# Performance work log

Hardware: AMD Instinct MI355X
Metric: run time of the kernel (lower is better)

Reference implementation:

```python
import jax, jax.numpy as jnp
import numpy as np

B, S, D = 4, 4096, 1024
H = 16
DH = D // H  # 64, required by the fused kernel


def setup_inputs() -> dict:
    key = jax.random.key(0)
    ks = jax.random.split(key, 5)
    scale = 1.0 / np.sqrt(D)  # xavier-ish init scale for square matrices
    return {
        "x": jax.random.normal(ks[0], (B, S, D), dtype=jnp.float32),
        "Wq": jax.random.normal(ks[1], (D, D), dtype=jnp.float32) * scale,
        "Wk": jax.random.normal(ks[2], (D, D), dtype=jnp.float32) * scale,
        "Wv": jax.random.normal(ks[3], (D, D), dtype=jnp.float32) * scale,
        "Wo": jax.random.normal(ks[4], (D, D), dtype=jnp.float32) * scale,
    }


def reference(x, Wq, Wk, Wv, Wo):
    # Fused QKV projection + linear (non-softmax) attention.
    # Q = x Wq, K = x Wk, V = x Wv, split into H heads of size DH.
    b, s, d = x.shape
    h, dh = H, d // H

    def to_heads(t):
        return t.reshape(b, s, h, dh).transpose(0, 2, 1, 3)  # [B,H,S,dh]

    q = to_heads(jnp.einsum("bsd,de->bse", x, Wq))
    k = to_heads(jnp.einsum("bsd,de->bse", x, Wk))
    v = to_heads(jnp.einsum("bsd,de->bse", x, Wv))

    # Linear attention: O(S * dh^2) per head, never materializes [S,S].
    # out = (1/sqrt(dh)) * Q @ (K^T V)
    scale = 1.0 / jnp.sqrt(jnp.asarray(dh, dtype=x.dtype))
    kv = jnp.einsum("bhsd,bhse->bhde", k, v)          # [B,H,dh,dh]
    out = jnp.einsum("bhsd,bhde->bhse", q, kv) * scale  # [B,H,S,dh]

    # kernel output [B,H,S,dh] -> transpose(1,2) -> view [B,S,D]
    out = out.transpose(0, 2, 1, 3).reshape(b, s, d)
    # out_proj: nn.Linear(D, D, bias=False) -> x @ W.T
    return jnp.einsum("bsd,ed->bse", out, Wo)
```

## Files before the change

### kernel.cpp

```cpp
#include <hip/hip_runtime.h>

typedef unsigned short u16;
typedef unsigned int u32;
typedef u16 u16x8 __attribute__((ext_vector_type(8)));
typedef u16 u16x4 __attribute__((ext_vector_type(4)));
typedef __bf16 bf16x8 __attribute__((ext_vector_type(8)));
typedef float f32x4 __attribute__((ext_vector_type(4)));

__device__ __forceinline__ u16 f2bf(float f) {
    u32 u = __builtin_bit_cast(u32, f);
    u32 r = (u + 0x7fffu + ((u >> 16) & 1u)) >> 16;
    return (u16)r;
}
__device__ __forceinline__ void async16(const u16* g, u16* lds_base) {
    __builtin_amdgcn_global_load_lds(
        (const __attribute__((address_space(1))) void*)g,
        (__attribute__((address_space(3))) void*)lds_base, 16, 0, 0);
}
template <bool SW>
__device__ __forceinline__ f32x4 mf(bf16x8 a, bf16x8 b, f32x4 c) {
    if constexpr (SW) return __builtin_amdgcn_mfma_f32_16x16x32_bf16(b, a, c, 0, 0, 0);
    else              return __builtin_amdgcn_mfma_f32_16x16x32_bf16(a, b, c, 0, 0, 0);
}

#define BAR __builtin_amdgcn_s_barrier()
#define WAITLGK do { asm volatile("s_waitcnt lgkmcnt(0)" ::: "memory"); \
                     __builtin_amdgcn_sched_barrier(0); } while (0)
#define PRIO1 __builtin_amdgcn_s_setprio(1)
#define PRIO0 __builtin_amdgcn_s_setprio(0)
#define VM(n) asm volatile("s_waitcnt vmcnt(" #n ")" ::: "memory")

__global__ void xpose_cvt(const float* __restrict__ x, u16* __restrict__ xb,
                          u16* __restrict__ xbT) {
    __shared__ u16 tile[32][33];
    const int s0 = blockIdx.y * 32, n0 = blockIdx.x * 32;
    const int tx = threadIdx.x, ty = threadIdx.y;
#pragma unroll
    for (int r = 0; r < 4; ++r) {
        const int s = s0 + ty + 8 * r;
        const u16 bv = f2bf(x[(size_t)s * 1024 + n0 + tx]);
        xb[(size_t)s * 1024 + n0 + tx] = bv;
        tile[ty + 8 * r][tx] = bv;
    }
    __syncthreads();
    const int b = s0 >> 12;
    const int sl = s0 & 4095;
#pragma unroll
    for (int r = 0; r < 4; ++r) {
        const int n = n0 + ty + 8 * r;
        xbT[((size_t)b * 1024 + n) * 4096 + sl + tx] = tile[tx][ty + 8 * r];
    }
}

__global__ void cvt2_f32_bf16(const float* __restrict__ wq, u16* __restrict__ wqb,
                              const float* __restrict__ wo, u16* __restrict__ wob) {
    const int bid = blockIdx.x;
    const float* src = bid < 512 ? wq : wo;
    u16* dst = bid < 512 ? wqb : wob;
    const long base = bid < 512 ? bid : bid - 512;
    const long idx = (base * 256 + threadIdx.x) * 8;
    float4 a = *(const float4*)(src + idx);
    float4 b = *(const float4*)(src + idx + 4);
    u16x8 o;
    o[0] = f2bf(a.x); o[1] = f2bf(a.y); o[2] = f2bf(a.z); o[3] = f2bf(a.w);
    o[4] = f2bf(b.x); o[5] = f2bf(b.y); o[6] = f2bf(b.z); o[7] = f2bf(b.w);
    *(u16x8*)(dst + idx) = o;
}

__global__ void transpose_cvt(const float* __restrict__ W0, const float* __restrict__ W1,
                              u16* __restrict__ WT) {
    __shared__ float tile[32][33];
    const float* W = (blockIdx.z == 0) ? W0 : W1;
    int n0 = blockIdx.x * 32, k0 = blockIdx.y * 32;
    int tx = threadIdx.x, ty = threadIdx.y;
#pragma unroll
    for (int r = 0; r < 4; ++r)
        tile[ty + 8 * r][tx] = W[(size_t)(k0 + ty + 8 * r) * 1024 + n0 + tx];
    __syncthreads();
#pragma unroll
    for (int r = 0; r < 4; ++r) {
        int n = n0 + ty + 8 * r;
        WT[((size_t)blockIdx.z * 1024 + n) * 1024 + k0 + tx] = f2bf(tile[tx][ty + 8 * r]);
    }
}

__global__ __launch_bounds__(512, 1) void gemmS(
    const u16* __restrict__ A, int lda,
    const u16* __restrict__ Bt, int ldb,
    u16* __restrict__ C, int ldc, int K, int nTN,
    size_t aMask, size_t btStrideB) {
    __shared__ u16 SM[4][2][128 * 64];
    const int tid = threadIdx.x, wid = tid >> 6, lane = tid & 63;
    const int wm = wid >> 2, wn = wid & 3;

    const int nwg = gridDim.x;
    const int orig = blockIdx.x;
    const int id = (orig & 7) * (nwg >> 3) + (orig >> 3);
    const size_t mBase = (size_t)(id / nTN) * 128;
    const size_t nBase = (size_t)(id % nTN) * 128;
    const size_t mA = mBase & aMask;
    Bt += (mBase >> 10) * btStrideB;

    const int srow = lane >> 3;
    const int scol = ((lane & 7) ^ (srow & 7)) * 8;

    auto stageS = [&](int buf, int kt) {
#pragma unroll
        for (int c = 0; c < 2; ++c) {
            const u16* g = c ? Bt : A;
            const int ld = c ? ldb : lda;
            const size_t rb = c ? nBase : mA;
            u16* lds = SM[buf][c];
#pragma unroll
            for (int j = 0; j < 2; ++j) {
                const int rowL = wid * 16 + j * 8;
                async16(g + (rb + rowL + srow) * (size_t)ld + (size_t)kt * 64 + scol,
                        lds + rowL * 64);
            }
        }
    };

    const int frow = lane & 15;
    const int xs0 = ((lane >> 4) ^ (frow & 7)) * 8;
    const int xs1 = ((4 + (lane >> 4)) ^ (frow & 7)) * 8;
    f32x4 acc[4][2] = {};

    const int nk = K >> 6;
    stageS(0, 0); stageS(1, 1); stageS(2, 2);
    VM(8);
    BAR;

    for (int kt = 0; kt < nk; ++kt) {
        const int cur = kt & 3;
        if (kt + 3 < nk) stageS((kt + 3) & 3, kt + 3);
        bf16x8 aF[4][2], bF[2][2];
#pragma unroll
        for (int mi = 0; mi < 4; ++mi) {
            const int rA = (wm * 64 + mi * 16 + frow) * 64;
            aF[mi][0] = *(const bf16x8*)&SM[cur][0][rA + xs0];
            aF[mi][1] = *(const bf16x8*)&SM[cur][0][rA + xs1];
        }
#pragma unroll
        for (int ni = 0; ni < 2; ++ni) {
            const int rB = (wn * 32 + ni * 16 + frow) * 64;
            bF[ni][0] = *(const bf16x8*)&SM[cur][1][rB + xs0];
            bF[ni][1] = *(const bf16x8*)&SM[cur][1][rB + xs1];
        }
        WAITLGK;
        PRIO1;
#pragma unroll
        for (int mi = 0; mi < 4; ++mi)
#pragma unroll
            for (int ni = 0; ni < 2; ++ni)
#pragma unroll
                for (int s = 0; s < 2; ++s)
                    acc[mi][ni] = mf<true>(aF[mi][s], bF[ni][s], acc[mi][ni]);
        PRIO0;
        if (kt + 3 < nk)      { VM(8); }
        else if (kt + 2 < nk) { VM(4); }
        else if (kt + 1 < nk) { VM(0); }
        BAR;
    }

    const int rb4 = (lane >> 4) * 4, cx = lane & 15;
#pragma unroll
    for (int mi = 0; mi < 4; ++mi) {
        const size_t row = mBase + wm * 64 + mi * 16 + cx;
#pragma unroll
        for (int ni = 0; ni < 2; ++ni) {
            const size_t col = nBase + wn * 32 + ni * 16 + rb4;
            u16x4 v;
            v[0] = f2bf(acc[mi][ni][0]); v[1] = f2bf(acc[mi][ni][1]);
            v[2] = f2bf(acc[mi][ni][2]); v[3] = f2bf(acc[mi][ni][3]);
            *(u16x4*)&C[row * (size_t)ldc + col] = v;
        }
    }
}

#define As SM[0]
#define Bs SM[1]

#define LDA(buf, mh) do { _Pragma("unroll") for (int mi = 0; mi < 4; ++mi) { \
    const int rA = (wm * 128 + (mh) * 64 + mi * 16 + frow) * 64; \
    aF[mi][0] = *(const bf16x8*)&As[buf][rA + xs0]; \
    aF[mi][1] = *(const bf16x8*)&As[buf][rA + xs1]; } } while (0)

#define LDB(buf, nh) do { _Pragma("unroll") for (int ni = 0; ni < 2; ++ni) { \
    const int rB = (wn * 64 + (nh) * 32 + ni * 16 + frow) * 64; \
    bF[(nh) * 2 + ni][0] = *(const bf16x8*)&Bs[buf][rB + xs0]; \
    bF[(nh) * 2 + ni][1] = *(const bf16x8*)&Bs[buf][rB + xs1]; } } while (0)

#define MFQ(mh, nh) do { _Pragma("unroll") for (int mi = 0; mi < 4; ++mi) \
  _Pragma("unroll") for (int ni = 0; ni < 2; ++ni) \
  _Pragma("unroll") for (int s = 0; s < 2; ++s) \
    acc[(mh) * 4 + mi][(nh) * 2 + ni] = mf<true>( \
        aF[mi][s], bF[(nh) * 2 + ni][s], acc[(mh) * 4 + mi][(nh) * 2 + ni]); } while (0)

#define TILE4(buf, S2, S3, S4, W1, W2, WV) \
  LDA(buf, 0); LDB(buf, 0); BAR; WAITLGK; PRIO1; MFQ(0, 0); PRIO0; W1; BAR; \
  LDB(buf, 1); S2; BAR; WAITLGK; PRIO1; MFQ(0, 1); PRIO0; W2; BAR; \
  LDA(buf, 1); S3; BAR; WAITLGK; PRIO1; MFQ(1, 1); PRIO0; BAR; \
  S4; BAR; WAITLGK; PRIO1; MFQ(1, 0); PRIO0; WV; BAR;

__global__ __launch_bounds__(512, 2) void gemm8p(
    const u16* __restrict__ A, int lda,
    const u16* __restrict__ Bt, int ldb,
    float* __restrict__ Cq, int ldc, int K, int nTN,
    size_t btStrideB) {
    __shared__ u16 SM[2][2][256 * 64];
    const int tid = threadIdx.x;
    const int wid = tid >> 6, lane = tid & 63;
    const int wm = wid >> 2, wn = wid & 3;

    const int nwg = gridDim.x;
    const int orig = blockIdx.x;
    const int id = (orig & 7) * (nwg >> 3) + (orig >> 3);
    const size_t mBase = (size_t)(id / nTN) * 256;
    const size_t nBase = (size_t)(id % nTN) * 256;

    Bt += (mBase >> 12) * btStrideB;

    const int srow = lane >> 3;
    const int scol = (((lane & 7) ^ (srow & 7)) * 8);

    auto stageH = [&](int buf, int isB, int h, int kt) {
        const u16* g = isB ? Bt : A;
        const int ld = isB ? ldb : lda;
        const size_t rb = isB ? nBase : mBase;
        u16* lds = isB ? Bs[buf] : As[buf];
#pragma unroll
        for (int j = 0; j < 2; ++j) {
            const int rowL = isB ? ((wid >> 1) * 64 + h * 32 + (wid & 1) * 16 + j * 8)
                                 : ((wid >> 2) * 128 + h * 64 + (wid & 3) * 16 + j * 8);
            async16(g + (rb + rowL + srow) * (size_t)ld + (size_t)kt * 64 + scol,
                    lds + rowL * 64);
        }
    };

    const int frow = lane & 15;
    const int xs0 = (((lane >> 4)) ^ (frow & 7)) * 8;
    const int xs1 = ((4 + (lane >> 4)) ^ (frow & 7)) * 8;

    f32x4 acc[8][4] = {};
    bf16x8 aF[4][2], bF[4][2];

#pragma unroll
    for (int h = 0; h < 2; ++h) { stageH(0, 0, h, 0); stageH(0, 1, h, 0); }
#pragma unroll
    for (int h = 0; h < 2; ++h) { stageH(1, 0, h, 1); stageH(1, 1, h, 1); }
    VM(8);
    BAR;

    const int np = K >> 7;
    for (int p = 0; p < np - 1; ++p) {
        const int k2 = 2 * p + 2, k3 = 2 * p + 3;
        TILE4(0,
              { stageH(0, 0, 0, k2); stageH(0, 1, 0, k2); },
              stageH(0, 1, 1, k2),
              stageH(0, 0, 1, k2),
              VM(10), VM(12), VM(12));
        TILE4(1,
              { stageH(1, 0, 0, k3); stageH(1, 1, 0, k3); },
              stageH(1, 1, 1, k3),
              stageH(1, 0, 1, k3),
              VM(10), VM(12), VM(12));
    }
    TILE4(0, , , , , , VM(0));
    TILE4(1, , , , , , );

    const int rb4 = (lane >> 4) * 4;
    const int cx = lane & 15;
#pragma unroll
    for (int m = 0; m < 8; ++m) {
        const size_t row = mBase + wm * 128 + m * 16 + cx;
#pragma unroll
        for (int n = 0; n < 4; ++n) {
            const size_t col = nBase + wn * 64 + n * 16 + rb4;
            *(float4*)&Cq[row * (size_t)ldc + col] = *(float4*)&acc[m][n];
        }
    }
}

__global__ __launch_bounds__(256, 2) void kv_small(
    const u16* __restrict__ M1v, const u16* __restrict__ WvT, u16* __restrict__ kvb) {
    __shared__ u16 Ks[64 * 64];
    __shared__ u16 Vs[64 * 64];
    const int h = blockIdx.x, b = blockIdx.y;
    const int tid = threadIdx.x, w = tid >> 6, lane = tid & 63;
    const int srow = lane >> 3;
    const int scol = ((lane & 7) ^ srow) * 8;
    const int frow = lane & 15;
    const int xs0 = ((lane >> 4) ^ (frow & 7)) * 8;
    const int xs1 = ((4 + (lane >> 4)) ^ (frow & 7)) * 8;
    const u16* Ap = M1v + (size_t)b * 1048576 + (size_t)h * 64 * 1024;
    const u16* Bp = WvT + (size_t)h * 64 * 1024;
    f32x4 acc[4] = {};
    for (int kk = 0; kk < 16; ++kk) {
        __syncthreads();
#pragma unroll
        for (int j = 0; j < 2; ++j) {
            const int row = w * 16 + j * 8;
            async16(Ap + (size_t)(row + srow) * 1024 + kk * 64 + scol, &Ks[row * 64]);
            async16(Bp + (size_t)(row + srow) * 1024 + kk * 64 + scol, &Vs[row * 64]);
        }
        VM(0);
        __syncthreads();
        bf16x8 a0 = *(const bf16x8*)&Ks[(w * 16 + frow) * 64 + xs0];
        bf16x8 a1 = *(const bf16x8*)&Ks[(w * 16 + frow) * 64 + xs1];
#pragma unroll
        for (int n = 0; n < 4; ++n) {
            bf16x8 b0 = *(const bf16x8*)&Vs[(n * 16 + frow) * 64 + xs0];
            bf16x8 b1 = *(const bf16x8*)&Vs[(n * 16 + frow) * 64 + xs1];
            acc[n] = mf<false>(a0, b0, acc[n]);
            acc[n] = mf<false>(a1, b1, acc[n]);
        }
    }
    const int rb4 = (lane >> 4) * 4, cx = lane & 15;
    u16* p = kvb + ((size_t)(b * 16 + h)) * 4096;
#pragma unroll
    for (int n = 0; n < 4; ++n)
#pragma unroll
        for (int r = 0; r < 4; ++r)
            p[(w * 16 + rb4 + r) * 64 + n * 16 + cx] = f2bf(acc[n][r] * 0.125f);
}

__global__ __launch_bounds__(256, 2) void w2_gemm(
    const u16* __restrict__ Wob, const u16* __restrict__ kvb, u16* __restrict__ W2t) {
    __shared__ u16 Aw[256 * 64];
    __shared__ u16 Bw[64 * 64];
    const int eT = blockIdx.x, h = blockIdx.y, b = blockIdx.z;
    const int tid = threadIdx.x, w = tid >> 6, lane = tid & 63;
    const int srow = lane >> 3;
    const int scol = ((lane & 7) ^ srow) * 8;
#pragma unroll
    for (int j = 0; j < 8; ++j) {
        const int row = w * 64 + j * 8;
        async16(Wob + (size_t)(eT * 256 + row + srow) * 1024 + h * 64 + scol, &Aw[row * 64]);
    }
#pragma unroll
    for (int j = 0; j < 2; ++j) {
        const int row = w * 16 + j * 8;
        async16(kvb + ((size_t)(b * 16 + h) * 64 + row + srow) * 64 + scol, &Bw[row * 64]);
    }
    VM(0);
    __syncthreads();
    const int frow = lane & 15;
    const int xs0 = ((lane >> 4) ^ (frow & 7)) * 8;
    const int xs1 = ((4 + (lane >> 4)) ^ (frow & 7)) * 8;
    f32x4 acc[4][4] = {};
#pragma unroll
    for (int m = 0; m < 4; ++m) {
        bf16x8 a0 = *(const bf16x8*)&Aw[(w * 64 + m * 16 + frow) * 64 + xs0];
        bf16x8 a1 = *(const bf16x8*)&Aw[(w * 64 + m * 16 + frow) * 64 + xs1];
#pragma unroll
        for (int n = 0; n < 4; ++n) {
            bf16x8 b0 = *(const bf16x8*)&Bw[(n * 16 + frow) * 64 + xs0];
            bf16x8 b1 = *(const bf16x8*)&Bw[(n * 16 + frow) * 64 + xs1];
            acc[m][n] = mf<false>(a0, b0, acc[m][n]);
            acc[m][n] = mf<false>(a1, b1, acc[m][n]);
        }
    }
    const int rb4 = (lane >> 4) * 4, cx = lane & 15;
    u16* out = W2t + (size_t)b * 1048576;
#pragma unroll
    for (int m = 0; m < 4; ++m)
#pragma unroll
        for (int n = 0; n < 4; ++n)
#pragma unroll
            for (int r = 0; r < 4; ++r)
                out[(size_t)(eT * 256 + w * 64 + m * 16 + rb4 + r) * 1024 + h * 64 + n * 16 + cx] =
                    f2bf(acc[m][n][r]);
}

extern "C" void kernel_launch(void* const* d_in, const int* in_sizes, int n_in,
                              void* d_out, int out_size, void* d_ws, size_t ws_size,
                              hipStream_t stream) {
    const float* x  = (const float*)d_in[0];
    const float* Wq = (const float*)d_in[1];
    const float* Wk = (const float*)d_in[2];
    const float* Wv = (const float*)d_in[3];
    const float* Wo = (const float*)d_in[4];
    float* out = (float*)d_out;
    char* ws = (char*)d_ws;

    u16* xb   = (u16*)(ws);
    u16* xbT  = (u16*)(ws + 33554432);
    u16* G    = (u16*)(ws + 67108864);
    u16* M1v  = (u16*)(ws + 75497472);
    u16* WkvT = (u16*)(ws + 83886080);
    u16* Wqb  = (u16*)(ws + 88080384);
    u16* Wob  = (u16*)(ws + 90177536);
    u16* kvb  = (u16*)(ws + 92274688);
    u16* W2t  = (u16*)(ws + 92798976);
    u16* W3T  = (u16*)(ws + 101187584);
    u16* WkT  = WkvT;
    u16* WvT  = WkvT + 1048576;

    xpose_cvt<<<dim3(32, 512), dim3(32, 8), 0, stream>>>(x, xb, xbT);
    cvt2_f32_bf16<<<1024, 256, 0, stream>>>(Wq, Wqb, Wo, Wob);
    transpose_cvt<<<dim3(32, 32, 2), dim3(32, 8), 0, stream>>>(Wk, Wv, WkvT);

    gemmS<<<256, 512, 0, stream>>>(xbT, 4096, xbT, 4096, G, 1024, 4096, 8,
                                   ~0ULL, 4194304ULL);
    gemmS<<<256, 512, 0, stream>>>(WkT, 1024, G, 1024, M1v, 1024, 1024, 8,
                                   1023ULL, 1048576ULL);
    kv_small<<<dim3(16, 4), 256, 0, stream>>>(M1v, WvT, kvb);
    w2_gemm<<<dim3(4, 16, 4), 256, 0, stream>>>(Wob, kvb, W2t);
    gemmS<<<256, 512, 0, stream>>>(W2t, 1024, Wqb, 1024, W3T, 1024, 1024, 8,
                                   ~0ULL, 0ULL);
    gemm8p<<<256, 512, 0, stream>>>(xb, 1024, W3T, 1024, out, 1024, 1024, 4, 1048576ULL);
}
```

Baseline: 157.7 us.

## Split K across two warp groups in gemmS with LDS reduction epilogue

Replaces gemmS with gemmS2, where the eight waves form two groups, each handling alternate 64-wide K slices of a paired stage. Each wave now computes a 64x64 sub-tile (4x4 MFMA accumulators) instead of 64x32, so more MFMAs are issued per LDS fragment load. The two partial sums are reduced through LDS in a swizzled epilogue before the bf16 store. The kernel also doubles register pressure per wave, declares launch_bounds(512,2), changes the pipeline to a two-deep paired buffer, and adds an extra barrier per iteration plus a reduction step.

New measurement: 157.0 us. About the same (-0.5%).

```diff
diff --git a/kernel.cpp b/kernel.cpp
--- a/kernel.cpp
+++ b/kernel.cpp
@@ -84,14 +84,14 @@
     }
 }
 
-__global__ __launch_bounds__(512, 1) void gemmS(
+__global__ __launch_bounds__(512, 2) void gemmS2(
     const u16* __restrict__ A, int lda,
     const u16* __restrict__ Bt, int ldb,
     u16* __restrict__ C, int ldc, int K, int nTN,
     size_t aMask, size_t btStrideB) {
-    __shared__ u16 SM[4][2][128 * 64];
+    __shared__ u16 SM[2][2][2][128 * 64];
     const int tid = threadIdx.x, wid = tid >> 6, lane = tid & 63;
-    const int wm = wid >> 2, wn = wid & 3;
+    const int wr = (wid >> 1) & 1, wc = wid & 1, grp = wid >> 2;
 
     const int nwg = gridDim.x;
     const int orig = blockIdx.x;
@@ -104,13 +104,13 @@
     const int srow = lane >> 3;
     const int scol = ((lane & 7) ^ (srow & 7)) * 8;
 
-    auto stageS = [&](int buf, int kt) {
+    auto stageT = [&](int pb, int sub, int kt) {
 #pragma unroll
         for (int c = 0; c < 2; ++c) {
             const u16* g = c ? Bt : A;
             const int ld = c ? ldb : lda;
             const size_t rb = c ? nBase : mA;
-            u16* lds = SM[buf][c];
+            u16* lds = SM[pb][sub][c];
 #pragma unroll
             for (int j = 0; j < 2; ++j) {
                 const int rowL = wid * 16 + j * 8;
@@ -123,56 +123,83 @@
     const int frow = lane & 15;
     const int xs0 = ((lane >> 4) ^ (frow & 7)) * 8;
     const int xs1 = ((4 + (lane >> 4)) ^ (frow & 7)) * 8;
-    f32x4 acc[4][2] = {};
+    f32x4 acc[4][4] = {};
 
     const int nk = K >> 6;
-    stageS(0, 0); stageS(1, 1); stageS(2, 2);
+    const int np2 = nk >> 1;
+    stageT(0, 0, 0); stageT(0, 1, 1);
+    stageT(1, 0, 2); stageT(1, 1, 3);
     VM(8);
     BAR;
 
-    for (int kt = 0; kt < nk; ++kt) {
-        const int cur = kt & 3;
-        if (kt + 3 < nk) stageS((kt + 3) & 3, kt + 3);
-        bf16x8 aF[4][2], bF[2][2];
+    for (int p = 0; p < np2; ++p) {
+        const int cur = p & 1;
+        const u16* Abuf = SM[cur][grp][0];
+        const u16* Bbuf = SM[cur][grp][1];
+        bf16x8 aF[4][2], bF[4][2];
 #pragma unroll
         for (int mi = 0; mi < 4; ++mi) {
-            const int rA = (wm * 64 + mi * 16 + frow) * 64;
-            aF[mi][0] = *(const bf16x8*)&SM[cur][0][rA + xs0];
-            aF[mi][1] = *(const bf16x8*)&SM[cur][0][rA + xs1];
-        }
-#pragma unroll
-        for (int ni = 0; ni < 2; ++ni) {
-            const int rB = (wn * 32 + ni * 16 + frow) * 64;
-            bF[ni][0] = *(const bf16x8*)&SM[cur][1][rB + xs0];
-            bF[ni][1] = *(const bf16x8*)&SM[cur][1][rB + xs1];
+            const int rA = (wr * 64 + mi * 16 + frow) * 64;
+            aF[mi][0] = *(const bf16x8*)&Abuf[rA + xs0];
+            aF[mi][1] = *(const bf16x8*)&Abuf[rA + xs1];
+        }
+#pragma unroll
+        for (int ni = 0; ni < 4; ++ni) {
+            const int rB = (wc * 64 + ni * 16 + frow) * 64;
+            bF[ni][0] = *(const bf16x8*)&Bbuf[rB + xs0];
+            bF[ni][1] = *(const bf16x8*)&Bbuf[rB + xs1];
         }
         WAITLGK;
         PRIO1;
 #pragma unroll
         for (int mi = 0; mi < 4; ++mi)
 #pragma unroll
-            for (int ni = 0; ni < 2; ++ni)
+            for (int ni = 0; ni < 4; ++ni)
 #pragma unroll
                 for (int s = 0; s < 2; ++s)
                     acc[mi][ni] = mf<true>(aF[mi][s], bF[ni][s], acc[mi][ni]);
         PRIO0;
-        if (kt + 3 < nk)      { VM(8); }
-        else if (kt + 2 < nk) { VM(4); }
-        else if (kt + 1 < nk) { VM(0); }
         BAR;
-    }
-
-    const int rb4 = (lane >> 4) * 4, cx = lane & 15;
-#pragma unroll
-    for (int mi = 0; mi < 4; ++mi) {
-        const size_t row = mBase + wm * 64 + mi * 16 + cx;
-#pragma unroll
-        for (int ni = 0; ni < 2; ++ni) {
-            const size_t col = nBase + wn * 32 + ni * 16 + rb4;
-            u16x4 v;
-            v[0] = f2bf(acc[mi][ni][0]); v[1] = f2bf(acc[mi][ni][1]);
-            v[2] = f2bf(acc[mi][ni][2]); v[3] = f2bf(acc[mi][ni][3]);
-            *(u16x4*)&C[row * (size_t)ldc + col] = v;
+        if (p + 2 < np2) {
+            stageT(cur, 0, 2 * (p + 2)); stageT(cur, 1, 2 * (p + 2) + 1);
+            VM(8);
+        } else if (p + 1 < np2) {
+            VM(0);
+        }
+        BAR;
+    }
+
+    float* R = (float*)&SM[0][0][0][0];
+    const int slot = wr * 2 + wc;
+    const int hi = lane >> 4, cx = lane & 15, rb4 = hi * 4;
+    if (grp == 1) {
+#pragma unroll
+        for (int mi = 0; mi < 4; ++mi) {
+            const int row = mi * 16 + cx;
+#pragma unroll
+            for (int ni = 0; ni < 4; ++ni) {
+                const int unit = (ni * 4 + hi) ^ cx;
+                *(f32x4*)((char*)R + slot * 16384 + row * 256 + unit * 16) = acc[mi][ni];
+            }
+        }
+    }
+    __syncthreads();
+    if (grp == 0) {
+#pragma unroll
+        for (int mi = 0; mi < 4; ++mi) {
+            const int rowL = mi * 16 + cx;
+            const size_t row = mBase + wr * 64 + rowL;
+#pragma unroll
+            for (int ni = 0; ni < 4; ++ni) {
+                const int unit = (ni * 4 + hi) ^ cx;
+                f32x4 o = *(const f32x4*)((char*)R + slot * 16384 + rowL * 256 + unit * 16);
+                f32x4 r = o + acc[mi][ni];
+                const size_t col = nBase + wc * 64 + ni * 16 + rb4;
+                u16x4 v;
+                v[0] = f2bf(r[0]); v[1] = f2bf(r[1]);
+                v[2] = f2bf(r[2]); v[3] = f2bf(r[3]);
+                *(u16x4*)&C[row * (size_t)ldc + col] = v;
+            }
         }
     }
 }
@@ -400,13 +427,13 @@
     cvt2_f32_bf16<<<1024, 256, 0, stream>>>(Wq, Wqb, Wo, Wob);
     transpose_cvt<<<dim3(32, 32, 2), dim3(32, 8), 0, stream>>>(Wk, Wv, WkvT);
 
-    gemmS<<<256, 512, 0, stream>>>(xbT, 4096, xbT, 4096, G, 1024, 4096, 8,
-                                   ~0ULL, 4194304ULL);
-    gemmS<<<256, 512, 0, stream>>>(WkT, 1024, G, 1024, M1v, 1024, 1024, 8,
-                                   1023ULL, 1048576ULL);
+    gemmS2<<<256, 512, 0, stream>>>(xbT, 4096, xbT, 4096, G, 1024, 4096, 8,
+                                    ~0ULL, 4194304ULL);
+    gemmS2<<<256, 512, 0, stream>>>(WkT, 1024, G, 1024, M1v, 1024, 1024, 8,
+                                    1023ULL, 1048576ULL);
     kv_small<<<dim3(16, 4), 256, 0, stream>>>(M1v, WvT, kvb);
     w2_gemm<<<dim3(4, 16, 4), 256, 0, stream>>>(Wob, kvb, W2t);
-    gemmS<<<256, 512, 0, stream>>>(W2t, 1024, Wqb, 1024, W3T, 1024, 1024, 8,
-                                   ~0ULL, 0ULL);
+    gemmS2<<<256, 512, 0, stream>>>(W2t, 1024, Wqb, 1024, W3T, 1024, 1024, 8,
+                                    ~0ULL, 0ULL);
     gemm8p<<<256, 512, 0, stream>>>(xb, 1024, W3T, 1024, out, 1024, 1024, 4, 1048576ULL);
 }
```

## Replace gemmS with smaller 128x64-tile gemmT for higher occupancy

Applied to the files above, without the earlier changes.

Replaces the 512-thread 128x128-tile GEMM, which used a four-stage LDS ring, with a 256-thread 128x64-tile kernel using double buffering. It launches twice as many blocks and allows up to three blocks per CU. The goal is more parallelism across CUs and more latency hiding through occupancy instead of deep prefetch. The costs are a shallower pipeline, a full vmcnt(0) wait every iteration, and more redundant A-tile reads from global memory.

Result: slower. 170.7 us (+8.2%).

```diff
diff --git a/kernel.cpp b/kernel.cpp
--- a/kernel.cpp
+++ b/kernel.cpp
@@ -84,39 +84,39 @@
     }
 }
 
-__global__ __launch_bounds__(512, 1) void gemmS(
+__global__ __launch_bounds__(256, 3) void gemmT(
     const u16* __restrict__ A, int lda,
     const u16* __restrict__ Bt, int ldb,
     u16* __restrict__ C, int ldc, int K, int nTN,
     size_t aMask, size_t btStrideB) {
-    __shared__ u16 SM[4][2][128 * 64];
-    const int tid = threadIdx.x, wid = tid >> 6, lane = tid & 63;
-    const int wm = wid >> 2, wn = wid & 3;
+    __shared__ u16 A2[2][128 * 64];
+    __shared__ u16 B2[2][64 * 64];
+    const int tid = threadIdx.x, w = tid >> 6, lane = tid & 63;
+    const int wr = w >> 1, wc = w & 1;
 
     const int nwg = gridDim.x;
     const int orig = blockIdx.x;
     const int id = (orig & 7) * (nwg >> 3) + (orig >> 3);
     const size_t mBase = (size_t)(id / nTN) * 128;
-    const size_t nBase = (size_t)(id % nTN) * 128;
+    const size_t nBase = (size_t)(id % nTN) * 64;
     const size_t mA = mBase & aMask;
     Bt += (mBase >> 10) * btStrideB;
 
     const int srow = lane >> 3;
-    const int scol = ((lane & 7) ^ (srow & 7)) * 8;
-
-    auto stageS = [&](int buf, int kt) {
-#pragma unroll
-        for (int c = 0; c < 2; ++c) {
-            const u16* g = c ? Bt : A;
-            const int ld = c ? ldb : lda;
-            const size_t rb = c ? nBase : mA;
-            u16* lds = SM[buf][c];
-#pragma unroll
-            for (int j = 0; j < 2; ++j) {
-                const int rowL = wid * 16 + j * 8;
-                async16(g + (rb + rowL + srow) * (size_t)ld + (size_t)kt * 64 + scol,
-                        lds + rowL * 64);
-            }
+    const int scol = ((lane & 7) ^ srow) * 8;
+
+    auto stage = [&](int buf, int kt) {
+#pragma unroll
+        for (int j = 0; j < 4; ++j) {
+            const int rowL = w * 32 + j * 8;
+            async16(A + (mA + rowL + srow) * (size_t)lda + (size_t)kt * 64 + scol,
+                    &A2[buf][rowL * 64]);
+        }
+#pragma unroll
+        for (int j = 0; j < 2; ++j) {
+            const int rowL = w * 16 + j * 8;
+            async16(Bt + (nBase + rowL + srow) * (size_t)ldb + (size_t)kt * 64 + scol,
+                    &B2[buf][rowL * 64]);
         }
     };
 
@@ -125,26 +125,25 @@
     const int xs1 = ((4 + (lane >> 4)) ^ (frow & 7)) * 8;
     f32x4 acc[4][2] = {};
 
+    stage(0, 0);
+    VM(0);
+    BAR;
     const int nk = K >> 6;
-    stageS(0, 0); stageS(1, 1); stageS(2, 2);
-    VM(8);
-    BAR;
-
     for (int kt = 0; kt < nk; ++kt) {
-        const int cur = kt & 3;
-        if (kt + 3 < nk) stageS((kt + 3) & 3, kt + 3);
+        const int cur = kt & 1;
+        if (kt + 1 < nk) stage(cur ^ 1, kt + 1);
         bf16x8 aF[4][2], bF[2][2];
 #pragma unroll
         for (int mi = 0; mi < 4; ++mi) {
-            const int rA = (wm * 64 + mi * 16 + frow) * 64;
-            aF[mi][0] = *(const bf16x8*)&SM[cur][0][rA + xs0];
-            aF[mi][1] = *(const bf16x8*)&SM[cur][0][rA + xs1];
+            const int rA = (wr * 64 + mi * 16 + frow) * 64;
+            aF[mi][0] = *(const bf16x8*)&A2[cur][rA + xs0];
+            aF[mi][1] = *(const bf16x8*)&A2[cur][rA + xs1];
         }
 #pragma unroll
         for (int ni = 0; ni < 2; ++ni) {
-            const int rB = (wn * 32 + ni * 16 + frow) * 64;
-            bF[ni][0] = *(const bf16x8*)&SM[cur][1][rB + xs0];
-            bF[ni][1] = *(const bf16x8*)&SM[cur][1][rB + xs1];
+            const int rB = (wc * 32 + ni * 16 + frow) * 64;
+            bF[ni][0] = *(const bf16x8*)&B2[cur][rB + xs0];
+            bF[ni][1] = *(const bf16x8*)&B2[cur][rB + xs1];
         }
         WAITLGK;
         PRIO1;
@@ -156,19 +155,17 @@
                 for (int s = 0; s < 2; ++s)
                     acc[mi][ni] = mf<true>(aF[mi][s], bF[ni][s], acc[mi][ni]);
         PRIO0;
-        if (kt + 3 < nk)      { VM(8); }
-        else if (kt + 2 < nk) { VM(4); }
-        else if (kt + 1 < nk) { VM(0); }
+        VM(0);
         BAR;
     }
 
     const int rb4 = (lane >> 4) * 4, cx = lane & 15;
 #pragma unroll
     for (int mi = 0; mi < 4; ++mi) {
-        const size_t row = mBase + wm * 64 + mi * 16 + cx;
+        const size_t row = mBase + wr * 64 + mi * 16 + cx;
 #pragma unroll
         for (int ni = 0; ni < 2; ++ni) {
-            const size_t col = nBase + wn * 32 + ni * 16 + rb4;
+            const size_t col = nBase + wc * 32 + ni * 16 + rb4;
             u16x4 v;
             v[0] = f2bf(acc[mi][ni][0]); v[1] = f2bf(acc[mi][ni][1]);
             v[2] = f2bf(acc[mi][ni][2]); v[3] = f2bf(acc[mi][ni][3]);
@@ -400,13 +397,13 @@
     cvt2_f32_bf16<<<1024, 256, 0, stream>>>(Wq, Wqb, Wo, Wob);
     transpose_cvt<<<dim3(32, 32, 2), dim3(32, 8), 0, stream>>>(Wk, Wv, WkvT);
 
-    gemmS<<<256, 512, 0, stream>>>(xbT, 4096, xbT, 4096, G, 1024, 4096, 8,
+    gemmT<<<512, 256, 0, stream>>>(xbT, 4096, xbT, 4096, G, 1024, 4096, 16,
                                    ~0ULL, 4194304ULL);
-    gemmS<<<256, 512, 0, stream>>>(WkT, 1024, G, 1024, M1v, 1024, 1024, 8,
+    gemmT<<<512, 256, 0, stream>>>(WkT, 1024, G, 1024, M1v, 1024, 1024, 16,
                                    1023ULL, 1048576ULL);
     kv_small<<<dim3(16, 4), 256, 0, stream>>>(M1v, WvT, kvb);
     w2_gemm<<<dim3(4, 16, 4), 256, 0, stream>>>(Wob, kvb, W2t);
-    gemmS<<<256, 512, 0, stream>>>(W2t, 1024, Wqb, 1024, W3T, 1024, 1024, 8,
+    gemmT<<<512, 256, 0, stream>>>(W2t, 1024, Wqb, 1024, W3T, 1024, 1024, 16,
                                    ~0ULL, 0ULL);
     gemm8p<<<256, 512, 0, stream>>>(xb, 1024, W3T, 1024, out, 1024, 1024, 4, 1048576ULL);
 }
```

## Compute only lower-triangle tiles of symmetric Gram GEMM and mirror

Applied to the files above, without the earlier changes.

The Gram matrix x^T x is symmetric per batch, so the GEMM now launches only the 36 lower-triangle 128x128 tiles per batch via a triangular tile index mapping. A new mirrorG kernel transposes each strictly-lower tile into its upper counterpart through LDS. This removes nearly half of the K=4096 GEMM work at the cost of an extra kernel launch and fewer blocks than CUs.

Measured after the change: 159.8 us. No clear change (+1.4%).

```diff
diff --git a/kernel.cpp b/kernel.cpp
--- a/kernel.cpp
+++ b/kernel.cpp
@@ -88,7 +88,7 @@
     const u16* __restrict__ A, int lda,
     const u16* __restrict__ Bt, int ldb,
     u16* __restrict__ C, int ldc, int K, int nTN,
-    size_t aMask, size_t btStrideB) {
+    size_t aMask, size_t btStrideB, int sym) {
     __shared__ u16 SM[4][2][128 * 64];
     const int tid = threadIdx.x, wid = tid >> 6, lane = tid & 63;
     const int wm = wid >> 2, wn = wid & 3;
@@ -96,8 +96,18 @@
     const int nwg = gridDim.x;
     const int orig = blockIdx.x;
     const int id = (orig & 7) * (nwg >> 3) + (orig >> 3);
-    const size_t mBase = (size_t)(id / nTN) * 128;
-    const size_t nBase = (size_t)(id % nTN) * 128;
+    size_t mBase, nBase;
+    if (sym) {
+        const int b = id / 36, p = id % 36;
+        int tm = 0;
+        while ((tm + 1) * (tm + 2) / 2 <= p) ++tm;
+        const int tn = p - tm * (tm + 1) / 2;
+        mBase = (size_t)b * 1024 + (size_t)tm * 128;
+        nBase = (size_t)tn * 128;
+    } else {
+        mBase = (size_t)(id / nTN) * 128;
+        nBase = (size_t)(id % nTN) * 128;
+    }
     const size_t mA = mBase & aMask;
     Bt += (mBase >> 10) * btStrideB;
 
@@ -174,6 +184,33 @@
             v[2] = f2bf(acc[mi][ni][2]); v[3] = f2bf(acc[mi][ni][3]);
             *(u16x4*)&C[row * (size_t)ldc + col] = v;
         }
+    }
+}
+
+__global__ __launch_bounds__(256) void mirrorG(u16* __restrict__ G) {
+    __shared__ u16 T[128][132];
+    const int p = blockIdx.x, b = blockIdx.y;
+    int tm = 1;
+    while (tm * (tm + 1) / 2 <= p) ++tm;
+    const int tn = p - tm * (tm - 1) / 2;
+    const int t = threadIdx.x;
+    const size_t base = (size_t)b * 1024;
+#pragma unroll
+    for (int pass = 0; pass < 8; ++pass) {
+        const int r = pass * 16 + (t >> 4);
+        const int c = (t & 15) * 8;
+        *(u16x8*)&T[r][c] =
+            *(const u16x8*)&G[(base + tm * 128 + r) * 1024 + tn * 128 + c];
+    }
+    __syncthreads();
+#pragma unroll
+    for (int pass = 0; pass < 8; ++pass) {
+        const int j = pass * 16 + (t >> 4);
+        const int i0 = (t & 15) * 8;
+        u16x8 v;
+#pragma unroll
+        for (int q = 0; q < 8; ++q) v[q] = T[i0 + q][j];
+        *(u16x8*)&G[(base + tn * 128 + j) * 1024 + tm * 128 + i0] = v;
     }
 }
 
@@ -400,13 +437,14 @@
     cvt2_f32_bf16<<<1024, 256, 0, stream>>>(Wq, Wqb, Wo, Wob);
     transpose_cvt<<<dim3(32, 32, 2), dim3(32, 8), 0, stream>>>(Wk, Wv, WkvT);
 
-    gemmS<<<256, 512, 0, stream>>>(xbT, 4096, xbT, 4096, G, 1024, 4096, 8,
-                                   ~0ULL, 4194304ULL);
+    gemmS<<<144, 512, 0, stream>>>(xbT, 4096, xbT, 4096, G, 1024, 4096, 8,
+                                   ~0ULL, 4194304ULL, 1);
+    mirrorG<<<dim3(28, 4), 256, 0, stream>>>(G);
     gemmS<<<256, 512, 0, stream>>>(WkT, 1024, G, 1024, M1v, 1024, 1024, 8,
-                                   1023ULL, 1048576ULL);
+                                   1023ULL, 1048576ULL, 0);
     kv_small<<<dim3(16, 4), 256, 0, stream>>>(M1v, WvT, kvb);
     w2_gemm<<<dim3(4, 16, 4), 256, 0, stream>>>(Wob, kvb, W2t);
     gemmS<<<256, 512, 0, stream>>>(W2t, 1024, Wqb, 1024, W3T, 1024, 1024, 8,
-                                   ~0ULL, 0ULL);
+                                   ~0ULL, 0ULL, 0);
     gemm8p<<<256, 512, 0, stream>>>(xb, 1024, W3T, 1024, out, 1024, 1024, 4, 1048576ULL);
 }
```
